# Kernel optimization log

Measured on AMD Instinct MI355X. Metric: run time of the kernel, lower is better.

## Reference

```python
import jax, jax.numpy as jnp
import numpy as np

NG, NF, NW = 5, 10, 4
STEP = 1 + NG + NF            # 16 signatures per writer
B = NW * STEP                 # 64
T, DFEAT = 512, 64
GAMMA = 5.0                   # SoftDTW gamma
BANDWIDTH = 0.1               # Sakoe-Chiba band (|i-j| <= 0.1 -> diagonal only)
INF = 1e7                     # finite 'infinity' to keep grads NaN-free
ALPHA, BETA, P_W, R_W = 0.5, 1.0, 0.1, 0.1
MARGIN_MAX, MARGIN_MIN = 1.0, 0.1
K_NUM, K_MUL = 5, 2.0
SIZ = NW * (NW + 1) // 2      # 10 (buffer size in original code)


def setup_inputs() -> dict:
    key = jax.random.key(0)
    k1, k2 = jax.random.split(key)
    data = jax.random.normal(k1, (B, T, DFEAT), dtype=jnp.float32)
    teacher_data = jax.random.normal(k2, (B, T, DFEAT), dtype=jnp.float32)
    # equal lengths: the bandwidth=0.1 band only admits the main diagonal,
    # so only equal-length pairs yield finite SoftDTW values.
    lens = jnp.full((B,), T, dtype=jnp.int32)
    return {"data": data, "lens": lens, "teacher_data": teacher_data}


def sq_dist(X, Y):
    # X: [P,N,d], Y: [P,M,d] -> [P,N,M] squared euclidean cost (SoftDTW default)
    x2 = jnp.sum(X * X, -1)[:, :, None]
    y2 = jnp.sum(Y * Y, -1)[:, None, :]
    return x2 + y2 - 2.0 * jnp.einsum('bid,bjd->bij', X, Y)


def softdtw_batch(Dmat):
    # Batched SoftDTW via anti-diagonal wavefront scan. Dmat: [P,N,N].
    Pn, N, _ = Dmat.shape
    i = jnp.arange(N)
    k = jnp.arange(2 * N - 1)[:, None]            # diagonal index
    j = k - i[None, :]                            # [2N-1, N]
    valid = (j >= 0) & (j < N)
    inband = valid & (jnp.abs(i[None, :] - j) <= BANDWIDTH)
    jc = jnp.clip(j, 0, N - 1)
    Dg = Dmat[:, i[None, :], jc]                  # [P, 2N-1, N] diag-gathered costs
    Dg = jnp.moveaxis(Dg, 1, 0)                   # [2N-1, P, N]

    def step(carry, xs):
        Rp, Rp2 = carry                           # diagonals k-1, k-2; [P,N]
        Dk, mk, kk = xs
        pad = jnp.full((Pn, 1), INF, Dk.dtype)
        above = jnp.concatenate([pad, Rp[:, :-1]], axis=1)   # R[i-1, j]
        left = Rp                                             # R[i, j-1]
        diag = jnp.concatenate([pad, Rp2[:, :-1]], axis=1)   # R[i-1, j-1]
        stacked = jnp.stack([above, left, diag], axis=0)
        smin = -GAMMA * jax.nn.logsumexp(-stacked / GAMMA, axis=0)
        Rk = Dk + smin
        Rk = jnp.where(kk == 0, Dk, Rk)           # R[0,0] = D[0,0]
        Rk = jnp.where(mk[None, :], Rk, INF)      # outside band -> INF
        return (Rk, Rp), None

    init = (jnp.full((Pn, N), INF, Dmat.dtype), jnp.full((Pn, N), INF, Dmat.dtype))
    (Rlast, _), _ = jax.lax.scan(step, init, (Dg, inband, jnp.arange(2 * N - 1)))
    return Rlast[:, N - 1]                        # R[N-1, N-1]


def mmd_loss(src, tgt):
    # Literal multi-kernel Gaussian MMD applied to 3D [n,T,d] inputs:
    # torch broadcasting of ((total[None]-total[:,None])**2).sum(2) -> [2n,2n,d]
    n = src.shape[0]
    total = jnp.concatenate([src, tgt], axis=0)   # [2n, T, d]
    sq = jnp.sum(total * total, axis=1)           # [2n, d]
    cross = jnp.einsum('atd,btd->abd', total, total)
    L2 = sq[:, None, :] + sq[None, :, :] - 2.0 * cross
    ns = 2 * n
    bw = jax.lax.stop_gradient(jnp.sum(L2)) / (ns * ns - ns)  # .data in torch
    bw = bw / (K_MUL ** (K_NUM // 2))
    kernels = sum(jnp.exp(-L2 / (bw * (K_MUL ** ii))) for ii in range(K_NUM))
    XX, YY = kernels[:n, :n], kernels[n:, n:]
    XY, YX = kernels[:n, n:], kernels[n:, :n]
    return jnp.mean(XX + YY - XY - YX)


def reference(data, lens, teacher_data):
    lens_f = lens.astype(data.dtype)
    widx = jnp.arange(NW) * STEP
    a_idx = jnp.repeat(widx, NG + NF)                                   # anchors
    o_idx = (widx[:, None] + 1 + jnp.arange(NG + NF)[None, :]).reshape(-1)
    # batch student + teacher pairs into one SoftDTW call: [2P, T, T]
    X = jnp.concatenate([data[a_idx], teacher_data[a_idx]], axis=0)
    Y = jnp.concatenate([data[o_idx], teacher_data[o_idx]], axis=0)
    sd = softdtw_batch(sq_dist(X, Y))
    denom = lens_f[a_idx] + lens_f[o_idx]
    Pn = NW * (NG + NF)
    d_s = (sd[:Pn] / denom).reshape(NW, NG + NF)
    d_t = (sd[Pn:] / denom).reshape(NW, NG + NF)
    dist_g, dist_n = d_s[:, :NG], d_s[:, NG:]
    dist_g_t, dist_n_t = d_t[:, :NG], d_t[:, NG:]

    # teacher-driven dynamic margin
    dists_t = jax.nn.relu(dist_n_t[:, :, None] - dist_g_t[:, None, :])  # [NW,NF,NG]
    mx = jnp.max(dists_t, axis=(1, 2), keepdims=True)
    fd = (MARGIN_MAX - MARGIN_MIN) / mx * dists_t + MARGIN_MIN
    lk = jax.nn.relu(dist_g[:, None, :] - dist_n[:, :, None] + fd)
    nz = jax.lax.stop_gradient(jnp.sum(lk != 0, axis=(1, 2))).astype(lk.dtype)
    lv = jnp.sum(lk, axis=(1, 2)) / (nz + 1.0)
    ca = jnp.mean(dist_g, axis=1)
    cb = jnp.mean(dist_n[:, :5], axis=1)
    intra = jnp.sum(dist_g - ca[:, None], axis=1)
    inter = jax.nn.relu(BETA - jnp.abs(ca - cb))
    total_loss = jnp.mean(lv + intra * P_W + inter * R_W)

    # MMD over writer pairs, excluding last 5 (random forgeries)
    groups = data.reshape(NW, STEP, T, DFEAT)[:, :STEP - 5]             # [NW,11,T,d]
    pairs = [(i, j) for i in range(NW) for j in range(1, NW) if i != j]
    src = jnp.stack([groups[i] for i, _ in pairs])
    tgt = jnp.stack([groups[j] for _, j in pairs])
    mmd_vals = jax.vmap(mmd_loss)(src, tgt)
    mmds = jnp.zeros((SIZ,), data.dtype).at[:len(pairs)].set(mmd_vals)
    mmd1 = jnp.max(mmds) * ALPHA
    return total_loss + mmd1
```

## Files before the change

kernel.cpp:

```cpp
#include <hip/hip_runtime.h>
#include <math.h>

#define T_LEN 512
#define DF 64
#define ROW_ELEMS (T_LEN * DF)
#define STEP_ 16
#define NROWS_G 44
#define GSTRIDE (NROWS_G * DF)
#define MAGIC 0x13579BDFu

__constant__ int c_PI[9] = {0, 0, 0, 1, 1, 2, 2, 3, 3};
__constant__ int c_PJ[9] = {1, 2, 3, 2, 3, 1, 3, 1, 2};

__device__ inline float blockSum(float v, float* tmp4) {
    #pragma unroll
    for (int off = 32; off > 0; off >>= 1) v += __shfl_down(v, off);
    if ((threadIdx.x & 63) == 0) tmp4[threadIdx.x >> 6] = v;
    __syncthreads();
    const float s = tmp4[0] + tmp4[1] + tmp4[2] + tmp4[3];
    __syncthreads();
    return s;
}

__device__ inline void waitFlag(unsigned* f) {
    while (__hip_atomic_load(f, __ATOMIC_RELAXED, __HIP_MEMORY_SCOPE_AGENT) != MAGIC)
        __builtin_amdgcn_s_sleep(1);
}
__device__ inline void setFlag(unsigned* f) {
    __threadfence();
    __hip_atomic_store(f, MAGIC, __ATOMIC_RELAXED, __HIP_MEMORY_SCOPE_AGENT);
}
__device__ inline float loadF(float* p) {
    return __hip_atomic_load(p, __ATOMIC_RELAXED, __HIP_MEMORY_SCOPE_AGENT);
}

__global__ __launch_bounds__(256) void k_fused(
    const float* __restrict__ data, const float* __restrict__ teacher,
    const int* __restrict__ lens,
    float* __restrict__ sd,
    float* __restrict__ G0,
    float* __restrict__ G1,
    float* __restrict__ partial,
    unsigned* __restrict__ flag1,
    unsigned* __restrict__ flag2,
    float* __restrict__ out)
{
    const int b = blockIdx.x;
    const int tid = threadIdx.x;

    __shared__ float red2[16][16][DF];
    __shared__ float redS[256];
    __shared__ float diagT[22 * DF];
    __shared__ float tmp4[4];
    __shared__ float fin[256];
    __shared__ float mmd9[9];
    __shared__ float sdl[120];

    if (b < 132) {
        const int tile = b >> 1, half = b & 1;
        int q = tile, ta = 0;
        while (q >= 11 - ta) { q -= 11 - ta; ta++; }
        const int tb = ta + q;
        const int ty = tid >> 4, dq = tid & 15;
        const int ua0 = ta * 4, ub0 = tb * 4;

        const float4* rA[4];
        const float4* rB[4];
        #pragma unroll
        for (int i = 0; i < 4; ++i) {
            const int ua = ua0 + i, ub = ub0 + i;
            rA[i] = (const float4*)(data + (size_t)((ua / 11) * STEP_ + (ua % 11)) * ROW_ELEMS);
            rB[i] = (const float4*)(data + (size_t)((ub / 11) * STEP_ + (ub % 11)) * ROW_ELEMS);
        }

        float acc[4][4][4];
        #pragma unroll
        for (int i = 0; i < 4; ++i)
            #pragma unroll
            for (int j = 0; j < 4; ++j)
                #pragma unroll
                for (int c = 0; c < 4; ++c) acc[i][j][c] = 0.f;

        const int tbase = half * 256 + ty;
        #pragma unroll 2
        for (int it = 0; it < 16; ++it) {
            const int t = tbase + it * 16;
            float4 av[4], bv[4];
            #pragma unroll
            for (int i = 0; i < 4; ++i) av[i] = rA[i][t * 16 + dq];
            #pragma unroll
            for (int j = 0; j < 4; ++j) bv[j] = rB[j][t * 16 + dq];
            #pragma unroll
            for (int i = 0; i < 4; ++i)
                #pragma unroll
                for (int j = 0; j < 4; ++j) {
                    acc[i][j][0] += av[i].x * bv[j].x;
                    acc[i][j][1] += av[i].y * bv[j].y;
                    acc[i][j][2] += av[i].z * bv[j].z;
                    acc[i][j][3] += av[i].w * bv[j].w;
                }
        }

        #pragma unroll
        for (int i = 0; i < 4; ++i)
            #pragma unroll
            for (int j = 0; j < 4; ++j)
                *(float4*)&red2[ty][i * 4 + j][dq * 4] =
                    make_float4(acc[i][j][0], acc[i][j][1], acc[i][j][2], acc[i][j][3]);
        __syncthreads();

        float* __restrict__ Gh = half ? G1 : G0;
        for (int o = tid; o < 1024; o += 256) {
            const int ij = o >> 6, d = o & 63;
            float s = 0.f;
            #pragma unroll
            for (int t2 = 0; t2 < 16; ++t2) s += red2[t2][ij][d];
            const int ua = ua0 + (ij >> 2), ub = ub0 + (ij & 3);
            Gh[(size_t)ua * GSTRIDE + ub * DF + d] = s;
            Gh[(size_t)ub * GSTRIDE + ua * DF + d] = s;
        }
    } else {
        const int bb = b - 132;
        const float* src = (bb < 60) ? data : teacher;
        const int p = bb % 60;
        const int w = p / 15, k = p % 15;
        const float4* A = (const float4*)(src + (size_t)(w * STEP_) * ROW_ELEMS);
        const float4* O = (const float4*)(src + (size_t)(w * STEP_ + 1 + k) * ROW_ELEMS);
        float acc = 0.f;
        #pragma unroll 4
        for (int i = tid; i < ROW_ELEMS / 4; i += 256) {
            float4 a = A[i], o = O[i];
            float dx = a.x - o.x, dy = a.y - o.y, dz = a.z - o.z, dw = a.w - o.w;
            acc += dx * dx + dy * dy + dz * dz + dw * dw;
        }
        redS[tid] = acc;
        __syncthreads();
        for (int s = 128; s > 0; s >>= 1) {
            if (tid < s) redS[tid] += redS[tid + s];
            __syncthreads();
        }
        if (tid == 0) sd[bb] = redS[0];
    }

    __syncthreads();
    if (tid == 0) setFlag(&flag1[b]);

    if (b >= 198 && b != 251) return;

    if (b < 198) {
        if (tid < 132) waitFlag(&flag1[tid]);
        __syncthreads();
        __threadfence();

        const int p = b / 22, aa = b % 22;
        const int gi = c_PI[p], gj = c_PJ[p];

        for (int e = tid; e < 22 * DF; e += 256) {
            const int bb = e >> 6, d2 = e & 63;
            const int ub = (bb < 11) ? gi * 11 + bb : gj * 11 + bb - 11;
            const size_t off = (size_t)ub * GSTRIDE + ub * DF + d2;
            diagT[e] = G0[off] + G1[off];
        }

        const float4* G0q = (const float4*)G0;
        const float4* G1q = (const float4*)G1;
        float gs = 0.f;
        for (int e = tid; e < 7744; e += 256) {
            const int f4 = e % 176;
            const int sp = (e / 176) & 1;
            const int a2 = e / 352;
            const int ua = (a2 < 11) ? gi * 11 + a2 : gj * 11 + a2 - 11;
            const int colbase = (sp ? gj : gi) * 11 * DF;
            const size_t qi = ((size_t)ua * GSTRIDE + colbase) / 4 + f4;
            const float4 v0 = G0q[qi], v1 = G1q[qi];
            gs += (v0.x + v1.x) + (v0.y + v1.y) + (v0.z + v1.z) + (v0.w + v1.w);
        }
        __syncthreads();

        float dsp = 0.f;
        for (int e = tid; e < 22 * DF; e += 256) dsp += diagT[e];

        const float sumG    = blockSum(gs,  tmp4);
        const float diagSum = blockSum(dsp, tmp4);

        const float bw = (44.f * diagSum - 2.f * sumG) / (462.f * 4.f);
        const float inv0 = 1.f / bw;

        const int ua = (aa < 11) ? gi * 11 + aa : gj * 11 + aa - 11;
        const bool sa = (aa < 11);
        const float4* cr0 = (const float4*)(G0 + (size_t)ua * GSTRIDE);
        const float4* cr1 = (const float4*)(G1 + (size_t)ua * GSTRIDE);
        const float4* dTq = (const float4*)diagT;

        float s2 = 0.f;
        for (int e = tid; e < 22 * 16; e += 256) {
            const int bb = e >> 4, dq = e & 15;
            const int ub = (bb < 11) ? gi * 11 + bb : gj * 11 + bb - 11;
            const float4 c0 = cr0[ub * 16 + dq], c1 = cr1[ub * 16 + dq];
            const float4 dB = dTq[e];
            const float4 dA = dTq[aa * 16 + dq];
            float l2[4];
            l2[0] = dA.x + dB.x - 2.f * (c0.x + c1.x);
            l2[1] = dA.y + dB.y - 2.f * (c0.y + c1.y);
            l2[2] = dA.z + dB.z - 2.f * (c0.z + c1.z);
            l2[3] = dA.w + dB.w - 2.f * (c0.w + c1.w);
            float kv = 0.f;
            #pragma unroll
            for (int c = 0; c < 4; ++c) {
                float inv = inv0;
                #pragma unroll
                for (int ii = 0; ii < 5; ++ii) { kv += __expf(-l2[c] * inv); inv *= 0.5f; }
            }
            s2 += ((bb < 11) == sa) ? kv : -kv;
        }
        const float rowSum = blockSum(s2, tmp4);

        if (tid == 0) {
            partial[b] = rowSum;
            setFlag(&flag2[b]);
        }
        return;
    }

    if (tid < 252) waitFlag(&flag1[tid]);
    if (tid < 198) waitFlag(&flag2[tid]);
    __syncthreads();
    __threadfence();

    fin[tid] = (tid < 198) ? loadF(&partial[tid]) : 0.f;
    if (tid < 120) sdl[tid] = loadF(&sd[tid]);
    __syncthreads();

    if (tid < 9) {
        float s = 0.f;
        #pragma unroll
        for (int k2 = 0; k2 < 22; ++k2) s += fin[tid * 22 + k2];
        mmd9[tid] = s / (121.f * 64.f);
    }
    __syncthreads();

    if (tid == 0) {
        float total = 0.f;
        for (int w = 0; w < 4; ++w) {
            float ds[15], dt[15];
            for (int k = 0; k < 15; ++k) {
                const float denom = (float)lens[w * STEP_] + (float)lens[w * STEP_ + 1 + k];
                ds[k] = sdl[w * 15 + k] / denom;
                dt[k] = sdl[60 + w * 15 + k] / denom;
            }
            float mx = 0.f;
            for (int i = 0; i < 10; ++i)
                for (int j = 0; j < 5; ++j) {
                    float v = dt[5 + i] - dt[j];
                    v = v > 0.f ? v : 0.f;
                    mx = fmaxf(mx, v);
                }
            const float scale = (1.0f - 0.1f) / mx;
            float sum_lk = 0.f, nz = 0.f;
            for (int i = 0; i < 10; ++i)
                for (int j = 0; j < 5; ++j) {
                    float v = dt[5 + i] - dt[j];
                    v = v > 0.f ? v : 0.f;
                    const float fd = scale * v + 0.1f;
                    float lk = ds[j] - ds[5 + i] + fd;
                    lk = lk > 0.f ? lk : 0.f;
                    sum_lk += lk;
                    if (lk != 0.f) nz += 1.f;
                }
            const float lv = sum_lk / (nz + 1.f);
            const float ca = (ds[0] + ds[1] + ds[2] + ds[3] + ds[4]) * 0.2f;
            const float cb = (ds[5] + ds[6] + ds[7] + ds[8] + ds[9]) * 0.2f;
            const float intra = (ds[0] - ca) + (ds[1] - ca) + (ds[2] - ca) + (ds[3] - ca) + (ds[4] - ca);
            float inter = 1.0f - fabsf(ca - cb);
            inter = inter > 0.f ? inter : 0.f;
            total += lv + intra * 0.1f + inter * 0.1f;
        }
        total *= 0.25f;

        float mmax = 0.f;
        for (int q2 = 0; q2 < 9; ++q2) mmax = fmaxf(mmax, mmd9[q2]);
        out[0] = total + 0.5f * mmax;
    }
}

extern "C" void kernel_launch(void* const* d_in, const int* in_sizes, int n_in,
                              void* d_out, int out_size, void* d_ws, size_t ws_size,
                              hipStream_t stream) {
    const float* data    = (const float*)d_in[0];
    const int*   lens    = (const int*)d_in[1];
    const float* teacher = (const float*)d_in[2];
    float* out = (float*)d_out;

    float*    sd      = (float*)d_ws;
    float*    G0      = sd + 128;
    float*    G1      = G0 + (size_t)NROWS_G * GSTRIDE;
    float*    partial = G1 + (size_t)NROWS_G * GSTRIDE;
    unsigned* flag1   = (unsigned*)(partial + 256);
    unsigned* flag2   = flag1 + 256;

    k_fused<<<252, 256, 0, stream>>>(data, teacher, lens, sd, G0, G1,
                                     partial, flag1, flag2, out);
}
```

Baseline: 120.1 us.

## Collapse per-row MMD blocks into one block per writer pair

Before, 198 blocks (9 writer pairs × 22 rows) each recomputed the pair's full bandwidth reduction over the Gram matrices and then evaluated one row of the multi-scale Gaussian kernel. Now 9 blocks each compute the bandwidth once and evaluate all 22 rows, writing the normalized per-pair MMD straight to workspace. The final block then waits on only 9 MMD flags plus the distance flags. This removes the 22-fold redundant Gram reads and the extra partial-sum reduction stage. In exchange, each of the 9 blocks must do 22 times more exp-heavy work serially, so far fewer CUs carry the critical path.

```diff
diff --git a/kernel.cpp b/kernel.cpp
--- a/kernel.cpp
+++ b/kernel.cpp
@@ -12,6 +12,18 @@
 __constant__ int c_PI[9] = {0, 0, 0, 1, 1, 2, 2, 3, 3};
 __constant__ int c_PJ[9] = {1, 2, 3, 2, 3, 1, 3, 1, 2};
 
+__device__ inline float loadF(float* p) {
+    return __hip_atomic_load(p, __ATOMIC_RELAXED, __HIP_MEMORY_SCOPE_AGENT);
+}
+__device__ inline void waitFlag(unsigned* f) {
+    while (__hip_atomic_load(f, __ATOMIC_RELAXED, __HIP_MEMORY_SCOPE_AGENT) != MAGIC)
+        __builtin_amdgcn_s_sleep(1);
+}
+__device__ inline void setFlag(unsigned* f) {
+    __threadfence();
+    __hip_atomic_store(f, MAGIC, __ATOMIC_RELAXED, __HIP_MEMORY_SCOPE_AGENT);
+}
+
 __device__ inline float blockSum(float v, float* tmp4) {
     #pragma unroll
     for (int off = 32; off > 0; off >>= 1) v += __shfl_down(v, off);
@@ -22,25 +34,13 @@
     return s;
 }
 
-__device__ inline void waitFlag(unsigned* f) {
-    while (__hip_atomic_load(f, __ATOMIC_RELAXED, __HIP_MEMORY_SCOPE_AGENT) != MAGIC)
-        __builtin_amdgcn_s_sleep(1);
-}
-__device__ inline void setFlag(unsigned* f) {
-    __threadfence();
-    __hip_atomic_store(f, MAGIC, __ATOMIC_RELAXED, __HIP_MEMORY_SCOPE_AGENT);
-}
-__device__ inline float loadF(float* p) {
-    return __hip_atomic_load(p, __ATOMIC_RELAXED, __HIP_MEMORY_SCOPE_AGENT);
-}
-
-__global__ __launch_bounds__(256) void k_fused(
+__global__ __launch_bounds__(256) void k_fused2(
     const float* __restrict__ data, const float* __restrict__ teacher,
     const int* __restrict__ lens,
     float* __restrict__ sd,
     float* __restrict__ G0,
     float* __restrict__ G1,
-    float* __restrict__ partial,
+    float* __restrict__ mmd9,
     unsigned* __restrict__ flag1,
     unsigned* __restrict__ flag2,
     float* __restrict__ out)
@@ -52,8 +52,7 @@
     __shared__ float redS[256];
     __shared__ float diagT[22 * DF];
     __shared__ float tmp4[4];
-    __shared__ float fin[256];
-    __shared__ float mmd9[9];
+    __shared__ float mmd9l[9];
     __shared__ float sdl[120];
 
     if (b < 132) {
@@ -145,15 +144,13 @@
     __syncthreads();
     if (tid == 0) setFlag(&flag1[b]);
 
-    if (b >= 198 && b != 251) return;
-
-    if (b < 198) {
+    if (b >= 132 && b < 141) {
+        const int pair = b - 132;
         if (tid < 132) waitFlag(&flag1[tid]);
         __syncthreads();
         __threadfence();
 
-        const int p = b / 22, aa = b % 22;
-        const int gi = c_PI[p], gj = c_PJ[p];
+        const int gi = c_PI[pair], gj = c_PJ[pair];
 
         for (int e = tid; e < 22 * DF; e += 256) {
             const int bb = e >> 6, d2 = e & 63;
@@ -186,18 +183,17 @@
         const float bw = (44.f * diagSum - 2.f * sumG) / (462.f * 4.f);
         const float inv0 = 1.f / bw;
 
-        const int ua = (aa < 11) ? gi * 11 + aa : gj * 11 + aa - 11;
-        const bool sa = (aa < 11);
-        const float4* cr0 = (const float4*)(G0 + (size_t)ua * GSTRIDE);
-        const float4* cr1 = (const float4*)(G1 + (size_t)ua * GSTRIDE);
         const float4* dTq = (const float4*)diagT;
-
         float s2 = 0.f;
-        for (int e = tid; e < 22 * 16; e += 256) {
-            const int bb = e >> 4, dq = e & 15;
+        for (int e = tid; e < 7744; e += 256) {
+            const int aa = e / 352;
+            const int rest = e % 352;
+            const int bb = rest >> 4, dq = rest & 15;
+            const int ua = (aa < 11) ? gi * 11 + aa : gj * 11 + aa - 11;
             const int ub = (bb < 11) ? gi * 11 + bb : gj * 11 + bb - 11;
-            const float4 c0 = cr0[ub * 16 + dq], c1 = cr1[ub * 16 + dq];
-            const float4 dB = dTq[e];
+            const size_t ci = ((size_t)ua * GSTRIDE) / 4 + ub * 16 + dq;
+            const float4 c0 = G0q[ci], c1 = G1q[ci];
+            const float4 dB = dTq[bb * 16 + dq];
             const float4 dA = dTq[aa * 16 + dq];
             float l2[4];
             l2[0] = dA.x + dB.x - 2.f * (c0.x + c1.x);
@@ -211,32 +207,26 @@
                 #pragma unroll
                 for (int ii = 0; ii < 5; ++ii) { kv += __expf(-l2[c] * inv); inv *= 0.5f; }
             }
-            s2 += ((bb < 11) == sa) ? kv : -kv;
-        }
-        const float rowSum = blockSum(s2, tmp4);
+            s2 += (((aa < 11) == (bb < 11)) ? kv : -kv);
+        }
+        const float pairSum = blockSum(s2, tmp4);
 
         if (tid == 0) {
-            partial[b] = rowSum;
-            setFlag(&flag2[b]);
+            mmd9[pair] = pairSum / (121.f * 64.f);
+            setFlag(&flag2[pair]);
         }
         return;
     }
 
-    if (tid < 252) waitFlag(&flag1[tid]);
-    if (tid < 198) waitFlag(&flag2[tid]);
+    if (b != 251) return;
+
+    if (tid < 120) waitFlag(&flag1[132 + tid]);
+    if (tid < 9)   waitFlag(&flag2[tid]);
     __syncthreads();
     __threadfence();
 
-    fin[tid] = (tid < 198) ? loadF(&partial[tid]) : 0.f;
-    if (tid < 120) sdl[tid] = loadF(&sd[tid]);
-    __syncthreads();
-
-    if (tid < 9) {
-        float s = 0.f;
-        #pragma unroll
-        for (int k2 = 0; k2 < 22; ++k2) s += fin[tid * 22 + k2];
-        mmd9[tid] = s / (121.f * 64.f);
-    }
+    if (tid < 9)   mmd9l[tid] = loadF(&mmd9[tid]);
+    if (tid < 120) sdl[tid]   = loadF(&sd[tid]);
     __syncthreads();
 
     if (tid == 0) {
@@ -278,7 +268,7 @@
         total *= 0.25f;
 
         float mmax = 0.f;
-        for (int q2 = 0; q2 < 9; ++q2) mmax = fmaxf(mmax, mmd9[q2]);
+        for (int q2 = 0; q2 < 9; ++q2) mmax = fmaxf(mmax, mmd9l[q2]);
         out[0] = total + 0.5f * mmax;
     }
 }
@@ -294,10 +284,10 @@
     float*    sd      = (float*)d_ws;
     float*    G0      = sd + 128;
     float*    G1      = G0 + (size_t)NROWS_G * GSTRIDE;
-    float*    partial = G1 + (size_t)NROWS_G * GSTRIDE;
-    unsigned* flag1   = (unsigned*)(partial + 256);
+    float*    mmd9    = G1 + (size_t)NROWS_G * GSTRIDE;
+    unsigned* flag1   = (unsigned*)(mmd9 + 16);
     unsigned* flag2   = flag1 + 256;
 
-    k_fused<<<252, 256, 0, stream>>>(data, teacher, lens, sd, G0, G1,
-                                     partial, flag1, flag2, out);
-}
+    k_fused2<<<252, 256, 0, stream>>>(data, teacher, lens, sd, G0, G1,
+                                      mmd9, flag1, flag2, out);
+}
```

Result: no change. 118.9 us (-1.0%).
